# Optimization experiments

Measured on AMD Instinct MI355X. Metric: run time of the kernel, lower is better.

The kernel has to match this reference:

```python
import jax, jax.numpy as jnp
import numpy as np

N = 50000          # nodes (num_sensors)
E = 600000         # edges
IN_DIM = 75        # 3 * 25
DIMS = [(75, 128), (128, 128), (128, 32)]  # (in, out) per layer: in->hidden->hidden->bottleneck


def setup_inputs() -> dict:
    key = jax.random.key(0)
    ks = jax.random.split(key, 4 + 5 * len(DIMS))
    inp = {
        "x": jax.random.normal(ks[0], (N, IN_DIM), dtype=jnp.float32),
        "edge_index": jax.random.randint(ks[1], (2, E), 0, N, dtype=jnp.int64),
        "weight": jax.random.uniform(ks[2], (E,), dtype=jnp.float32),
        "sim": jax.random.normal(ks[3], (E, 2), dtype=jnp.float32),
    }
    i = 4
    for l, (cin, cout) in enumerate(DIMS):
        s = jnp.float32(1.0 / np.sqrt(cin))
        inp[f"wr{l}"] = jax.random.normal(ks[i + 0], (cin, cout), dtype=jnp.float32) * s  # real part of complex conv filter
        inp[f"wi{l}"] = jax.random.normal(ks[i + 1], (cin, cout), dtype=jnp.float32) * s  # imag part
        inp[f"cb{l}"] = jnp.zeros((cout,), dtype=jnp.float32)                              # conv bias
        inp[f"lw{l}"] = jax.random.normal(ks[i + 2], (cout, cin), dtype=jnp.float32) * s  # Linear weight (torch layout [out,in])
        inp[f"lb{l}"] = jnp.zeros((cout,), dtype=jnp.float32)                              # Linear bias
        i += 5
    return inp


def _layer(x, src, dst, cr, ci, wr, wi, cb, lw, lb):
    # ModeConvFast: gather source features, scale by complex edge coefficient
    # c = weight * (sim_r + i*sim_i), scatter-add to destination nodes,
    # project with complex filter W = wr + i*wi, keep real part, add bias.
    xs = x[src]                                   # [E, Cin] gather
    agg_r = jax.ops.segment_sum(xs * cr[:, None], dst, num_segments=N)  # [N, Cin]
    agg_i = jax.ops.segment_sum(xs * ci[:, None], dst, num_segments=N)  # [N, Cin]
    conv = agg_r @ wr - agg_i @ wi + cb           # real part of complex matmul
    return jax.nn.relu(conv + x @ lw.T + lb)      # conv(x,...) + lin(x), then relu


def reference(x, edge_index, weight, sim,
              wr0, wi0, cb0, lw0, lb0,
              wr1, wi1, cb1, lw1, lb1,
              wr2, wi2, cb2, lw2, lb2):
    src, dst = edge_index[0], edge_index[1]
    cr = weight * sim[:, 0]                       # [E] real edge coefficient
    ci = weight * sim[:, 1]                       # [E] imag edge coefficient
    layers = [
        (wr0, wi0, cb0, lw0, lb0),
        (wr1, wi1, cb1, lw1, lb1),
        (wr2, wi2, cb2, lw2, lb2),
    ]
    for p in layers:
        x = _layer(x, src, dst, cr, ci, *p)
    return x
```

## Files before the change

kernel.cpp:

```cpp
#include <hip/hip_runtime.h>

#define N_NODES 50000
#define N_EDGES 600000
#define E_PAD_MAX (N_EDGES + N_NODES * 7)

using bf16x8 = __attribute__((ext_vector_type(8))) short;
using f32x4  = __attribute__((ext_vector_type(4))) float;
typedef unsigned int uint32_tt;

__device__ __forceinline__ unsigned short f2bf(float f) {
    union { float f; unsigned int u; } v; v.f = f;
    unsigned int u = v.u;
    return (unsigned short)((u + 0x7fffu + ((u >> 16) & 1u)) >> 16);
}
__device__ __forceinline__ float bf2f(unsigned int h16) {
    union { unsigned int u; float f; } v; v.u = h16 << 16;
    return v.f;
}

__global__ void prep_kernel(
    const float* __restrict__ x0, unsigned short* __restrict__ xb,
    const float* __restrict__ wr0, const float* __restrict__ wi0,
    const float* __restrict__ lw0, unsigned short* __restrict__ BT0,
    const float* __restrict__ wr1, const float* __restrict__ wi1,
    const float* __restrict__ lw1, unsigned short* __restrict__ BT1,
    const float* __restrict__ wr2, const float* __restrict__ wi2,
    const float* __restrict__ lw2, unsigned short* __restrict__ BT2,
    int* __restrict__ cnt, uint2* __restrict__ edat, int n) {
    int tid = blockIdx.x * 256 + threadIdx.x;
    int nth = gridDim.x * 256;
    for (int i = tid; i < N_NODES; i += nth) cnt[i] = 0;
    uint2 z; z.x = 0u; z.y = 0u;
    for (int i = tid; i < E_PAD_MAX; i += nth) edat[i] = z;

    int i = tid;
    int nconv = n * 96;
    if (i < nconv) {
        int r = i / 96, c = i - r * 96;
        xb[i] = (c < 75) ? f2bf(x0[r * 75 + c]) : (unsigned short)0;
        return;
    }
    i -= nconv;
    if (i < 128 * 288) {
        int nn = i / 288, k = i - nn * 288;
        int part = k / 96, kk = k - part * 96;
        float v = 0.f;
        if (kk < 75) {
            if (part == 0)      v = wr0[kk * 128 + nn];
            else if (part == 1) v = -wi0[kk * 128 + nn];
            else                v = lw0[nn * 75 + kk];
        }
        BT0[i] = f2bf(v);
        return;
    }
    i -= 128 * 288;
    if (i < 128 * 384) {
        int nn = i / 384, k = i - nn * 384;
        int part = k >> 7, kk = k & 127;
        float v;
        if (part == 0)      v = wr1[kk * 128 + nn];
        else if (part == 1) v = -wi1[kk * 128 + nn];
        else                v = lw1[nn * 128 + kk];
        BT1[i] = f2bf(v);
        return;
    }
    i -= 128 * 384;
    if (i < 96 * 128) {
        int nn = i >> 7, k = i & 127;
        float v;
        if (nn < 32)      v = wr2[k * 32 + nn];
        else if (nn < 64) v = -wi2[k * 32 + (nn - 32)];
        else              v = lw2[(nn - 64) * 128 + k];
        BT2[i] = f2bf(v);
    }
}


__global__ void hist_kernel(const int* __restrict__ ei, int* __restrict__ cnt,
                            int* __restrict__ rank, int E) {
    int e = blockIdx.x * 256 + threadIdx.x;
    if (e < E) rank[e] = atomicAdd(&cnt[ei[E + e]], 1);
}

__global__ void scan1(const int* __restrict__ deg, int* __restrict__ out,
                      int* __restrict__ bsum, int n) {
    __shared__ int s[256];
    int t = threadIdx.x;
    int base = blockIdx.x * 1024 + t * 4;
    int v0 = (base + 0 < n) ? ((deg[base + 0] + 7) & ~7) : 0;
    int v1 = (base + 1 < n) ? ((deg[base + 1] + 7) & ~7) : 0;
    int v2 = (base + 2 < n) ? ((deg[base + 2] + 7) & ~7) : 0;
    int v3 = (base + 3 < n) ? ((deg[base + 3] + 7) & ~7) : 0;
    int tsum = v0 + v1 + v2 + v3;
    s[t] = tsum;
    __syncthreads();
    for (int off = 1; off < 256; off <<= 1) {
        int tmp = (t >= off) ? s[t - off] : 0;
        __syncthreads();
        s[t] += tmp;
        __syncthreads();
    }
    int excl = s[t] - tsum;
    if (base + 0 < n) out[base + 0] = excl;
    if (base + 1 < n) out[base + 1] = excl + v0;
    if (base + 2 < n) out[base + 2] = excl + v0 + v1;
    if (base + 3 < n) out[base + 3] = excl + v0 + v1 + v2;
    if (t == 255) bsum[blockIdx.x] = s[255];
}

__global__ void scan3(int* __restrict__ off, const int* __restrict__ bsum,
                      int n, int nb) {
    __shared__ int sp;
    int b = blockIdx.x, t = threadIdx.x;
    int seg = b >> 2;
    if (t == 0) {
        int acc = 0;
        for (int k = 0; k < seg; ++k) acc += bsum[k];
        sp = acc;
    }
    __syncthreads();
    int i = b * 256 + t;
    if (i < n) off[i] += sp;
    if (i == n) {
        int tot = sp;
        for (int k = seg; k < nb; ++k) tot += bsum[k];
        off[n] = tot;
    }
}

__global__ void scatter_kernel(const int* __restrict__ ei, const float* __restrict__ w,
                               const float* __restrict__ sim, const int* __restrict__ off,
                               const int* __restrict__ rank, uint2* __restrict__ edat,
                               int E) {
    int e = blockIdx.x * 256 + threadIdx.x;
    if (e >= E) return;
    int s = ei[e], d = ei[E + e];
    int p = off[d] + rank[e];
    float wt = w[e];
    uint2 m;
    m.x = (unsigned)s;
    m.y = (uint32_tt)f2bf(wt * sim[2 * e]) |
          ((uint32_tt)f2bf(wt * sim[2 * e + 1]) << 16);
    edat[p] = m;
}

template <int CU2>
__global__ __launch_bounds__(256) void agg_bf16(
    const uint32_tt* __restrict__ x, const int* __restrict__ off,
    const uint2* __restrict__ edat, uint32_tt* __restrict__ aggR,
    uint32_tt* __restrict__ aggI, int n) {
    int wave = threadIdx.x >> 6;
    int lane = threadIdx.x & 63;
    int node = __builtin_amdgcn_readfirstlane(blockIdx.x * 4 + wave);
    if (node >= n) return;
    int lc = (CU2 == 64) ? lane : (lane < CU2 ? lane : CU2 - 1);
    float arl = 0.f, arh = 0.f, ail = 0.f, aih = 0.f;
    int e0 = __builtin_amdgcn_readfirstlane(off[node]);
    int e1 = __builtin_amdgcn_readfirstlane(off[node + 1]);

    if (e0 < e1) {
        uint2 mn[8];
        int sc[8]; float crc[8], cic[8];
        uint32_tt wc[8];
        {
            uint2 m0[8];
#pragma unroll
            for (int j = 0; j < 8; ++j) m0[j] = edat[e0 + j];
#pragma unroll
            for (int j = 0; j < 8; ++j) {
                sc[j] = __builtin_amdgcn_readfirstlane((int)m0[j].x);
                int pk = __builtin_amdgcn_readfirstlane((int)m0[j].y);
                crc[j] = bf2f((unsigned)pk & 0xffffu);
                cic[j] = bf2f((unsigned)pk >> 16);
            }
            int nb = (e0 + 8 < e1) ? e0 + 8 : e0;
#pragma unroll
            for (int j = 0; j < 8; ++j) mn[j] = edat[nb + j];
#pragma unroll
            for (int j = 0; j < 8; ++j) wc[j] = x[(size_t)sc[j] * CU2 + lc];
        }
        for (int e = e0;; e += 8) {
            bool more = (e + 8 < e1);
            int sn[8]; float crn[8], cin_[8]; uint32_tt wn[8];
            if (more) {
#pragma unroll
                for (int j = 0; j < 8; ++j) {
                    sn[j] = __builtin_amdgcn_readfirstlane((int)mn[j].x);
                    int pk = __builtin_amdgcn_readfirstlane((int)mn[j].y);
                    crn[j] = bf2f((unsigned)pk & 0xffffu);
                    cin_[j] = bf2f((unsigned)pk >> 16);
                }
                int nb = (e + 16 < e1) ? e + 16 : e + 8;
#pragma unroll
                for (int j = 0; j < 8; ++j) mn[j] = edat[nb + j];
#pragma unroll
                for (int j = 0; j < 8; ++j) wn[j] = x[(size_t)sn[j] * CU2 + lc];
            }
#pragma unroll
            for (int j = 0; j < 8; ++j) {
                float lo = bf2f(wc[j] & 0xffffu), hi = bf2f(wc[j] >> 16);
                arl += crc[j] * lo; arh += crc[j] * hi;
                ail += cic[j] * lo; aih += cic[j] * hi;
            }
            if (!more) break;
#pragma unroll
            for (int j = 0; j < 8; ++j) {
                sc[j] = sn[j]; crc[j] = crn[j]; cic[j] = cin_[j]; wc[j] = wn[j];
            }
        }
    }
    if (lane < CU2) {
        aggR[(size_t)node * CU2 + lane] = (uint32_tt)f2bf(arl) | ((uint32_tt)f2bf(arh) << 16);
        aggI[(size_t)node * CU2 + lane] = (uint32_tt)f2bf(ail) | ((uint32_tt)f2bf(aih) << 16);
    }
}

__global__ __launch_bounds__(256) void agg_out(
    const uint32_tt* __restrict__ Y, const int* __restrict__ off,
    const uint2* __restrict__ edat, const float* __restrict__ cb,
    const float* __restrict__ lb, float* __restrict__ out, int n) {
    int wave = threadIdx.x >> 6;
    int lane = threadIdx.x & 63;
    int node = __builtin_amdgcn_readfirstlane(blockIdx.x * 4 + wave);
    if (node >= n) return;
    int lc = (lane < 32) ? lane : 31;
    int usei = (lane >> 4) & 1;
    float alo = 0.f, ahi = 0.f;
    int e0 = __builtin_amdgcn_readfirstlane(off[node]);
    int e1 = __builtin_amdgcn_readfirstlane(off[node + 1]);

    if (e0 < e1) {
        uint2 mn[8];
        int sc[8]; float crc[8], cic[8];
        uint32_tt wc[8];
        {
            uint2 m0[8];
#pragma unroll
            for (int j = 0; j < 8; ++j) m0[j] = edat[e0 + j];
#pragma unroll
            for (int j = 0; j < 8; ++j) {
                sc[j] = __builtin_amdgcn_readfirstlane((int)m0[j].x);
                int pk = __builtin_amdgcn_readfirstlane((int)m0[j].y);
                crc[j] = bf2f((unsigned)pk & 0xffffu);
                cic[j] = bf2f((unsigned)pk >> 16);
            }
            int nb = (e0 + 8 < e1) ? e0 + 8 : e0;
#pragma unroll
            for (int j = 0; j < 8; ++j) mn[j] = edat[nb + j];
#pragma unroll
            for (int j = 0; j < 8; ++j) wc[j] = Y[(size_t)sc[j] * 48 + lc];
        }
        for (int e = e0;; e += 8) {
            bool more = (e + 8 < e1);
            int sn[8]; float crn[8], cin_[8]; uint32_tt wn[8];
            if (more) {
#pragma unroll
                for (int j = 0; j < 8; ++j) {
                    sn[j] = __builtin_amdgcn_readfirstlane((int)mn[j].x);
                    int pk = __builtin_amdgcn_readfirstlane((int)mn[j].y);
                    crn[j] = bf2f((unsigned)pk & 0xffffu);
                    cin_[j] = bf2f((unsigned)pk >> 16);
                }
                int nb = (e + 16 < e1) ? e + 16 : e + 8;
#pragma unroll
                for (int j = 0; j < 8; ++j) mn[j] = edat[nb + j];
#pragma unroll
                for (int j = 0; j < 8; ++j) wn[j] = Y[(size_t)sn[j] * 48 + lc];
            }
#pragma unroll
            for (int j = 0; j < 8; ++j) {
                float c = usei ? cic[j] : crc[j];
                float lo = bf2f(wc[j] & 0xffffu), hi = bf2f(wc[j] >> 16);
                alo += c * lo; ahi += c * hi;
            }
            if (!more) break;
#pragma unroll
            for (int j = 0; j < 8; ++j) {
                sc[j] = sn[j]; crc[j] = crn[j]; cic[j] = cin_[j]; wc[j] = wn[j];
            }
        }
    }
    alo += __shfl_xor(alo, 16);
    ahi += __shfl_xor(ahi, 16);
    if (lane < 16) {
        uint32_tt lin = Y[(size_t)node * 48 + 32 + lane];
        int c0 = 2 * lane, c1 = 2 * lane + 1;
        float v0 = alo + bf2f(lin & 0xffffu) + cb[c0] + lb[c0];
        float v1 = ahi + bf2f(lin >> 16) + cb[c1] + lb[c1];
        float2 r;
        r.x = v0 > 0.f ? v0 : 0.f;
        r.y = v1 > 0.f ? v1 : 0.f;
        ((float2*)out)[(size_t)node * 16 + lane] = r;
    }
}

template <int CINP, int COUT, int BM, int WM, int WN, int MT, int NT,
          bool OUT_BF16, bool RAW, int PARTS>
__global__ __launch_bounds__(256) void gemm_mfma(
    const unsigned short* __restrict__ A0, const unsigned short* __restrict__ A1,
    const unsigned short* __restrict__ A2, const unsigned short* __restrict__ BT,
    const float* __restrict__ cb, const float* __restrict__ lb,
    void* __restrict__ outv, int n) {
    constexpr int PK = 40;
    constexpr int KTOT = PARTS * CINP;
    constexpr int NCH = KTOT / 32;
    constexpr int CPP = CINP / 32;
    __shared__ unsigned short sA[BM][PK];
    __shared__ unsigned short sB[COUT][PK];

    int t = threadIdx.x;
    int lane = t & 63, wave = t >> 6;
    int wm = wave / WN, wn = wave % WN;
    int ml = lane & 15, kh = lane >> 4;
    int node0 = blockIdx.x * BM;

    const unsigned short* Asrc[3] = {A0, A1, A2};

    f32x4 acc[MT][NT];
#pragma unroll
    for (int mt = 0; mt < MT; ++mt)
#pragma unroll
        for (int nt = 0; nt < NT; ++nt) acc[mt][nt] = (f32x4){0.f, 0.f, 0.f, 0.f};

    for (int c = 0; c < NCH; ++c) {
        int part = (PARTS == 1) ? 0 : (c / CPP);
        int kk = (c - part * CPP) * 32;
        const unsigned short* __restrict__ Ap = Asrc[part];
        __syncthreads();
#pragma unroll
        for (int i = t; i < BM * 4; i += 256) {
            int r = i >> 2, q = i & 3;
            int node = node0 + r;
            if (node >= n) node = n - 1;
            *(uint4*)&sA[r][q * 8] =
                *(const uint4*)(Ap + (size_t)node * CINP + kk + q * 8);
        }
#pragma unroll
        for (int i = t; i < COUT * 4; i += 256) {
            int r = i >> 2, q = i & 3;
            *(uint4*)&sB[r][q * 8] =
                *(const uint4*)(BT + (size_t)r * KTOT + c * 32 + q * 8);
        }
        __syncthreads();
        bf16x8 af[MT], bfr[NT];
#pragma unroll
        for (int mt = 0; mt < MT; ++mt)
            af[mt] = *(const bf16x8*)&sA[wm * (MT * 16) + mt * 16 + ml][kh * 8];
#pragma unroll
        for (int nt = 0; nt < NT; ++nt)
            bfr[nt] = *(const bf16x8*)&sB[wn * (NT * 16) + nt * 16 + ml][kh * 8];
#pragma unroll
        for (int mt = 0; mt < MT; ++mt)
#pragma unroll
            for (int nt = 0; nt < NT; ++nt)
                acc[mt][nt] = __builtin_amdgcn_mfma_f32_16x16x32_bf16(
                    af[mt], bfr[nt], acc[mt][nt], 0, 0, 0);
    }

    int row0 = kh * 4;
#pragma unroll
    for (int nt = 0; nt < NT; ++nt) {
        int col = wn * (NT * 16) + nt * 16 + ml;
        float bias = RAW ? 0.f : (cb[col] + lb[col]);
#pragma unroll
        for (int mt = 0; mt < MT; ++mt) {
#pragma unroll
            for (int r = 0; r < 4; ++r) {
                int node = node0 + wm * (MT * 16) + mt * 16 + row0 + r;
                if (node < n) {
                    float v = acc[mt][nt][r] + bias;
                    if (!RAW) v = v > 0.f ? v : 0.f;
                    if (OUT_BF16)
                        ((unsigned short*)outv)[(size_t)node * COUT + col] = f2bf(v);
                    else
                        ((float*)outv)[(size_t)node * COUT + col] = v;
                }
            }
        }
    }
}

__global__ __launch_bounds__(256) void gemm_l1y(
    const unsigned short* __restrict__ A0, const unsigned short* __restrict__ A1,
    const unsigned short* __restrict__ A2, const unsigned short* __restrict__ BT,
    const unsigned short* __restrict__ BT2, const float* __restrict__ cb,
    const float* __restrict__ lb, unsigned short* __restrict__ Yout, int n) {
    constexpr int PK = 40;
    constexpr int PH = 136;
    __shared__ unsigned short sA[128][PK];
    __shared__ unsigned short sB[128][PK];
    __shared__ unsigned short sH[128][PH];

    int t = threadIdx.x;
    int lane = t & 63, wave = t >> 6;
    int wm = wave >> 1, wn = wave & 1;
    int ml = lane & 15, kh = lane >> 4;
    int node0 = blockIdx.x * 128;
    const unsigned short* Asrc[3] = {A0, A1, A2};

    f32x4 acc[4][4];
#pragma unroll
    for (int mt = 0; mt < 4; ++mt)
#pragma unroll
        for (int nt = 0; nt < 4; ++nt) acc[mt][nt] = (f32x4){0.f, 0.f, 0.f, 0.f};

    for (int c = 0; c < 12; ++c) {
        int part = c >> 2;
        int kk = (c & 3) * 32;
        const unsigned short* __restrict__ Ap = Asrc[part];
        __syncthreads();
#pragma unroll
        for (int i = t; i < 512; i += 256) {
            int r = i >> 2, q = i & 3;
            int node = node0 + r;
            if (node >= n) node = n - 1;
            *(uint4*)&sA[r][q * 8] =
                *(const uint4*)(Ap + (size_t)node * 128 + kk + q * 8);
        }
#pragma unroll
        for (int i = t; i < 512; i += 256) {
            int r = i >> 2, q = i & 3;
            *(uint4*)&sB[r][q * 8] =
                *(const uint4*)(BT + (size_t)r * 384 + c * 32 + q * 8);
        }
        __syncthreads();
        bf16x8 af[4], bfr[4];
#pragma unroll
        for (int mt = 0; mt < 4; ++mt)
            af[mt] = *(const bf16x8*)&sA[wm * 64 + mt * 16 + ml][kh * 8];
#pragma unroll
        for (int nt = 0; nt < 4; ++nt)
            bfr[nt] = *(const bf16x8*)&sB[wn * 64 + nt * 16 + ml][kh * 8];
#pragma unroll
        for (int mt = 0; mt < 4; ++mt)
#pragma unroll
            for (int nt = 0; nt < 4; ++nt)
                acc[mt][nt] = __builtin_amdgcn_mfma_f32_16x16x32_bf16(
                    af[mt], bfr[nt], acc[mt][nt], 0, 0, 0);
    }

    int row0 = kh * 4;
#pragma unroll
    for (int nt = 0; nt < 4; ++nt) {
        int col = wn * 64 + nt * 16 + ml;
        float bias = cb[col] + lb[col];
#pragma unroll
        for (int mt = 0; mt < 4; ++mt) {
#pragma unroll
            for (int r = 0; r < 4; ++r) {
                int nl = wm * 64 + mt * 16 + row0 + r;
                float v = acc[mt][nt][r] + bias;
                sH[nl][col] = f2bf(v > 0.f ? v : 0.f);
            }
        }
    }
    __syncthreads();

    f32x4 acc2[4][3];
#pragma unroll
    for (int mt = 0; mt < 4; ++mt)
#pragma unroll
        for (int nt = 0; nt < 3; ++nt) acc2[mt][nt] = (f32x4){0.f, 0.f, 0.f, 0.f};
    for (int c2 = 0; c2 < 4; ++c2) {
        bf16x8 af[4], bfr[3];
#pragma unroll
        for (int mt = 0; mt < 4; ++mt)
            af[mt] = *(const bf16x8*)&sH[wm * 64 + mt * 16 + ml][c2 * 32 + kh * 8];
#pragma unroll
        for (int nt = 0; nt < 3; ++nt) {
            int ycol = wn * 48 + nt * 16 + ml;
            bfr[nt] = *(const bf16x8*)(BT2 + (size_t)ycol * 128 + c2 * 32 + kh * 8);
        }
#pragma unroll
        for (int mt = 0; mt < 4; ++mt)
#pragma unroll
            for (int nt = 0; nt < 3; ++nt)
                acc2[mt][nt] = __builtin_amdgcn_mfma_f32_16x16x32_bf16(
                    af[mt], bfr[nt], acc2[mt][nt], 0, 0, 0);
    }
#pragma unroll
    for (int nt = 0; nt < 3; ++nt) {
        int ycol = wn * 48 + nt * 16 + ml;
#pragma unroll
        for (int mt = 0; mt < 4; ++mt) {
#pragma unroll
            for (int r = 0; r < 4; ++r) {
                int node = node0 + wm * 64 + mt * 16 + row0 + r;
                if (node < n)
                    Yout[(size_t)node * 96 + ycol] = f2bf(acc2[mt][nt][r]);
            }
        }
    }
}


extern "C" void kernel_launch(void* const* d_in, const int* in_sizes, int n_in,
                              void* d_out, int out_size, void* d_ws, size_t ws_size,
                              hipStream_t stream) {
    const float* x0  = (const float*)d_in[0];
    const int*   ei  = (const int*)d_in[1];
    const float* wgt = (const float*)d_in[2];
    const float* sim = (const float*)d_in[3];
    const float *wr[3], *wi[3], *cb[3], *lw[3], *lb[3];
    for (int l = 0; l < 3; ++l) {
        wr[l] = (const float*)d_in[4 + 5 * l];
        wi[l] = (const float*)d_in[5 + 5 * l];
        cb[l] = (const float*)d_in[6 + 5 * l];
        lw[l] = (const float*)d_in[7 + 5 * l];
        lb[l] = (const float*)d_in[8 + 5 * l];
    }

    char* p = (char*)d_ws;
    auto alloc = [&](size_t bytes) -> void* {
        void* r = p;
        p += (bytes + 255) & ~(size_t)255;
        return r;
    };
    int*   off  = (int*)alloc((N_NODES + 1) * 4);
    int*   cnt  = (int*)alloc(N_NODES * 4);
    int*   bsum = (int*)alloc(256);
    int*   rank = (int*)alloc((size_t)N_EDGES * 4);
    uint2* edat = (uint2*)alloc((size_t)E_PAD_MAX * 8);
    unsigned short* xb    = (unsigned short*)alloc((size_t)N_NODES * 96 * 2);
    unsigned short* aggRb = (unsigned short*)alloc((size_t)N_NODES * 128 * 2);
    unsigned short* aggIb = (unsigned short*)alloc((size_t)N_NODES * 128 * 2);
    unsigned short* h1b   = (unsigned short*)alloc((size_t)N_NODES * 128 * 2);
    unsigned short* Yb    = (unsigned short*)alloc((size_t)N_NODES * 96 * 2);
    unsigned short* BT0   = (unsigned short*)alloc((size_t)128 * 288 * 2);
    unsigned short* BT1   = (unsigned short*)alloc((size_t)128 * 384 * 2);
    unsigned short* BT2   = (unsigned short*)alloc((size_t)96 * 128 * 2);
    float* outp = (float*)d_out;

    {
        int total = N_NODES * 96 + 128 * 288 + 128 * 384 + 96 * 128;
        prep_kernel<<<(total + 255) / 256, 256, 0, stream>>>(
            x0, xb, wr[0], wi[0], lw[0], BT0, wr[1], wi[1], lw[1], BT1,
            wr[2], wi[2], lw[2], BT2, cnt, edat, N_NODES);
    }
    hist_kernel<<<(N_EDGES + 255) / 256, 256, 0, stream>>>(ei, cnt, rank, N_EDGES);
    int nb = (N_NODES + 1023) / 1024;
    scan1<<<nb, 256, 0, stream>>>(cnt, off, bsum, N_NODES);
    scan3<<<(N_NODES + 1 + 255) / 256, 256, 0, stream>>>(off, bsum, N_NODES, nb);
    scatter_kernel<<<(N_EDGES + 255) / 256, 256, 0, stream>>>(ei, wgt, sim, off, rank,
                                                              edat, N_EDGES);

    int agrid = (N_NODES + 3) / 4;

    agg_bf16<48><<<agrid, 256, 0, stream>>>((const uint32_tt*)xb, off, edat,
                                            (uint32_tt*)aggRb, (uint32_tt*)aggIb, N_NODES);
    gemm_mfma<96, 128, 128, 2, 2, 4, 4, true, false, 3>
        <<<(N_NODES + 127) / 128, 256, 0, stream>>>(aggRb, aggIb, xb, BT0, cb[0], lb[0],
                                                    h1b, N_NODES);
    agg_bf16<64><<<agrid, 256, 0, stream>>>((const uint32_tt*)h1b, off, edat,
                                            (uint32_tt*)aggRb, (uint32_tt*)aggIb, N_NODES);
    gemm_l1y<<<(N_NODES + 127) / 128, 256, 0, stream>>>(aggRb, aggIb, h1b, BT1, BT2,
                                                        cb[1], lb[1], Yb, N_NODES);
    agg_out<<<agrid, 256, 0, stream>>>((const uint32_tt*)Yb, off, edat, cb[2], lb[2],
                                       outp, N_NODES);
}
```

Measured before the change: 263.3 us.

## Store features in 32-channel planes and split aggregation across channel chunks

Feature, aggregate and Y buffers move from node-major rows to planar blocks of 32 bf16 channels per node, and the GEMM loads and stores follow the new layout. Aggregation kernels now handle one 32-channel plane per wave, with four edges processed in parallel across lane groups and combined by shuffle reductions. Block indices are interleaved so the chunks of the same nodes run close together. This is meant to make each gathered row a compact 64-byte segment and to spread edge latency across more waves, at the cost of reading the edge list once per chunk plus extra shuffles.

Result: slower. 385.5 us (+46.4%).

```diff
diff --git a/kernel.cpp b/kernel.cpp
--- a/kernel.cpp
+++ b/kernel.cpp
@@ -7,6 +7,7 @@
 using bf16x8 = __attribute__((ext_vector_type(8))) short;
 using f32x4  = __attribute__((ext_vector_type(4))) float;
 typedef unsigned int uint32_tt;
+typedef unsigned long long u64;
 
 __device__ __forceinline__ unsigned short f2bf(float f) {
     union { float f; unsigned int u; } v; v.f = f;
@@ -37,7 +38,8 @@
     int nconv = n * 96;
     if (i < nconv) {
         int r = i / 96, c = i - r * 96;
-        xb[i] = (c < 75) ? f2bf(x0[r * 75 + c]) : (unsigned short)0;
+        unsigned short v = (c < 75) ? f2bf(x0[r * 75 + c]) : (unsigned short)0;
+        xb[((size_t)(c >> 5) * n + r) * 32 + (c & 31)] = v;
         return;
     }
     i -= nconv;
@@ -144,74 +146,68 @@
     edat[p] = m;
 }
 
-template <int CU2>
-__global__ __launch_bounds__(256) void agg_bf16(
-    const uint32_tt* __restrict__ x, const int* __restrict__ off,
-    const uint2* __restrict__ edat, uint32_tt* __restrict__ aggR,
-    uint32_tt* __restrict__ aggI, int n) {
+template <int TOTCH>
+__global__ __launch_bounds__(256) void agg_ch(
+    const uint32_tt* __restrict__ x,
+    const int* __restrict__ off, const uint2* __restrict__ edat,
+    uint32_tt* __restrict__ aggR, uint32_tt* __restrict__ aggI, int n) {
+    static_assert(TOTCH == 3 || TOTCH == 4, "chunk count");
     int wave = threadIdx.x >> 6;
     int lane = threadIdx.x & 63;
-    int node = __builtin_amdgcn_readfirstlane(blockIdx.x * 4 + wave);
+    int bx = blockIdx.x;
+    int x8 = bx & 7, nbk = bx >> 3;
+    int chunk, node_blk;
+    if (TOTCH == 4) {
+        chunk = x8 >> 1;
+        node_blk = nbk * 2 + (x8 & 1);
+    } else {
+        if (x8 < 3)      { chunk = 0; node_blk = nbk * 3 + x8; }
+        else if (x8 < 6) { chunk = 1; node_blk = nbk * 3 + (x8 - 3); }
+        else             { chunk = 2; node_blk = nbk * 2 + (x8 - 6); }
+    }
+    int node = __builtin_amdgcn_readfirstlane(node_blk * 4 + wave);
     if (node >= n) return;
-    int lc = (CU2 == 64) ? lane : (lane < CU2 ? lane : CU2 - 1);
+    int j = lane >> 4;
+    int c = lane & 15;
+    const uint32_tt* __restrict__ xp = x + (size_t)chunk * n * 16;
     float arl = 0.f, arh = 0.f, ail = 0.f, aih = 0.f;
     int e0 = __builtin_amdgcn_readfirstlane(off[node]);
     int e1 = __builtin_amdgcn_readfirstlane(off[node + 1]);
 
     if (e0 < e1) {
-        uint2 mn[8];
-        int sc[8]; float crc[8], cic[8];
-        uint32_tt wc[8];
-        {
-            uint2 m0[8];
-#pragma unroll
-            for (int j = 0; j < 8; ++j) m0[j] = edat[e0 + j];
-#pragma unroll
-            for (int j = 0; j < 8; ++j) {
-                sc[j] = __builtin_amdgcn_readfirstlane((int)m0[j].x);
-                int pk = __builtin_amdgcn_readfirstlane((int)m0[j].y);
-                crc[j] = bf2f((unsigned)pk & 0xffffu);
-                cic[j] = bf2f((unsigned)pk >> 16);
+        const u64* __restrict__ ed64 = (const u64*)edat;
+        u64 mc = __builtin_nontemporal_load(ed64 + e0 + j);
+        int nb1 = (e0 + 4 < e1) ? e0 + 4 : e0;
+        u64 mn = __builtin_nontemporal_load(ed64 + nb1 + j);
+        uint32_tt wc = xp[(size_t)((uint32_tt)mc) * 16 + c];
+        for (int e = e0;; e += 4) {
+            bool more = (e + 4 < e1);
+            u64 mn2 = 0; uint32_tt wn = 0;
+            if (more) {
+                wn = xp[(size_t)((uint32_tt)mn) * 16 + c];
+                int nb2 = (e + 8 < e1) ? e + 8 : e + 4;
+                mn2 = __builtin_nontemporal_load(ed64 + nb2 + j);
             }
-            int nb = (e0 + 8 < e1) ? e0 + 8 : e0;
-#pragma unroll
-            for (int j = 0; j < 8; ++j) mn[j] = edat[nb + j];
-#pragma unroll
-            for (int j = 0; j < 8; ++j) wc[j] = x[(size_t)sc[j] * CU2 + lc];
-        }
-        for (int e = e0;; e += 8) {
-            bool more = (e + 8 < e1);
-            int sn[8]; float crn[8], cin_[8]; uint32_tt wn[8];
-            if (more) {
-#pragma unroll
-                for (int j = 0; j < 8; ++j) {
-                    sn[j] = __builtin_amdgcn_readfirstlane((int)mn[j].x);
-                    int pk = __builtin_amdgcn_readfirstlane((int)mn[j].y);
-                    crn[j] = bf2f((unsigned)pk & 0xffffu);
-                    cin_[j] = bf2f((unsigned)pk >> 16);
-                }
-                int nb = (e + 16 < e1) ? e + 16 : e + 8;
-#pragma unroll
-                for (int j = 0; j < 8; ++j) mn[j] = edat[nb + j];
-#pragma unroll
-                for (int j = 0; j < 8; ++j) wn[j] = x[(size_t)sn[j] * CU2 + lc];
-            }
-#pragma unroll
-            for (int j = 0; j < 8; ++j) {
-                float lo = bf2f(wc[j] & 0xffffu), hi = bf2f(wc[j] >> 16);
-                arl += crc[j] * lo; arh += crc[j] * hi;
-                ail += cic[j] * lo; aih += cic[j] * hi;
-            }
+            uint32_tt pk = (uint32_tt)(mc >> 32);
+            float cr = bf2f(pk & 0xffffu);
+            float ci = bf2f(pk >> 16);
+            float lo = bf2f(wc & 0xffffu), hi = bf2f(wc >> 16);
+            arl += cr * lo; arh += cr * hi;
+            ail += ci * lo; aih += ci * hi;
             if (!more) break;
-#pragma unroll
-            for (int j = 0; j < 8; ++j) {
-                sc[j] = sn[j]; crc[j] = crn[j]; cic[j] = cin_[j]; wc[j] = wn[j];
-            }
-        }
-    }
-    if (lane < CU2) {
-        aggR[(size_t)node * CU2 + lane] = (uint32_tt)f2bf(arl) | ((uint32_tt)f2bf(arh) << 16);
-        aggI[(size_t)node * CU2 + lane] = (uint32_tt)f2bf(ail) | ((uint32_tt)f2bf(aih) << 16);
+            mc = mn; mn = mn2; wc = wn;
+        }
+    }
+    arl += __shfl_xor(arl, 16); arl += __shfl_xor(arl, 32);
+    arh += __shfl_xor(arh, 16); arh += __shfl_xor(arh, 32);
+    ail += __shfl_xor(ail, 16); ail += __shfl_xor(ail, 32);
+    aih += __shfl_xor(aih, 16); aih += __shfl_xor(aih, 32);
+    if (lane < 16) {
+        size_t base = ((size_t)chunk * n + node) * 16 + lane;
+        __builtin_nontemporal_store(
+            (uint32_tt)f2bf(arl) | ((uint32_tt)f2bf(arh) << 16), aggR + base);
+        __builtin_nontemporal_store(
+            (uint32_tt)f2bf(ail) | ((uint32_tt)f2bf(aih) << 16), aggI + base);
     }
 }
 
@@ -223,67 +219,51 @@
     int lane = threadIdx.x & 63;
     int node = __builtin_amdgcn_readfirstlane(blockIdx.x * 4 + wave);
     if (node >= n) return;
-    int lc = (lane < 32) ? lane : 31;
-    int usei = (lane >> 4) & 1;
+    int j = lane >> 5;
+    int lc = lane & 31;
+    int p = lc >> 4;
+    int w = lc & 15;
+    const uint32_tt* __restrict__ Yp = Y + (size_t)p * n * 16;
     float alo = 0.f, ahi = 0.f;
     int e0 = __builtin_amdgcn_readfirstlane(off[node]);
     int e1 = __builtin_amdgcn_readfirstlane(off[node + 1]);
 
     if (e0 < e1) {
-        uint2 mn[8];
-        int sc[8]; float crc[8], cic[8];
-        uint32_tt wc[8];
-        {
-            uint2 m0[8];
-#pragma unroll
-            for (int j = 0; j < 8; ++j) m0[j] = edat[e0 + j];
-#pragma unroll
-            for (int j = 0; j < 8; ++j) {
-                sc[j] = __builtin_amdgcn_readfirstlane((int)m0[j].x);
-                int pk = __builtin_amdgcn_readfirstlane((int)m0[j].y);
-                crc[j] = bf2f((unsigned)pk & 0xffffu);
-                cic[j] = bf2f((unsigned)pk >> 16);
+        const u64* __restrict__ ed64 = (const u64*)edat;
+        u64 mcA = __builtin_nontemporal_load(ed64 + e0 + j);
+        u64 mcB = __builtin_nontemporal_load(ed64 + e0 + 2 + j);
+        int nb1 = (e0 + 4 < e1) ? e0 + 4 : e0;
+        u64 mnA = __builtin_nontemporal_load(ed64 + nb1 + j);
+        u64 mnB = __builtin_nontemporal_load(ed64 + nb1 + 2 + j);
+        uint32_tt wcA = Yp[(size_t)((uint32_tt)mcA) * 16 + w];
+        uint32_tt wcB = Yp[(size_t)((uint32_tt)mcB) * 16 + w];
+        for (int e = e0;; e += 4) {
+            bool more = (e + 4 < e1);
+            u64 mnA2 = 0, mnB2 = 0; uint32_tt wnA = 0, wnB = 0;
+            if (more) {
+                wnA = Yp[(size_t)((uint32_tt)mnA) * 16 + w];
+                wnB = Yp[(size_t)((uint32_tt)mnB) * 16 + w];
+                int nb2 = (e + 8 < e1) ? e + 8 : e + 4;
+                mnA2 = __builtin_nontemporal_load(ed64 + nb2 + j);
+                mnB2 = __builtin_nontemporal_load(ed64 + nb2 + 2 + j);
             }
-            int nb = (e0 + 8 < e1) ? e0 + 8 : e0;
-#pragma unroll
-            for (int j = 0; j < 8; ++j) mn[j] = edat[nb + j];
-#pragma unroll
-            for (int j = 0; j < 8; ++j) wc[j] = Y[(size_t)sc[j] * 48 + lc];
-        }
-        for (int e = e0;; e += 8) {
-            bool more = (e + 8 < e1);
-            int sn[8]; float crn[8], cin_[8]; uint32_tt wn[8];
-            if (more) {
-#pragma unroll
-                for (int j = 0; j < 8; ++j) {
-                    sn[j] = __builtin_amdgcn_readfirstlane((int)mn[j].x);
-                    int pk = __builtin_amdgcn_readfirstlane((int)mn[j].y);
-                    crn[j] = bf2f((unsigned)pk & 0xffffu);
-                    cin_[j] = bf2f((unsigned)pk >> 16);
-                }
-                int nb = (e + 16 < e1) ? e + 16 : e + 8;
-#pragma unroll
-                for (int j = 0; j < 8; ++j) mn[j] = edat[nb + j];
-#pragma unroll
-                for (int j = 0; j < 8; ++j) wn[j] = Y[(size_t)sn[j] * 48 + lc];
-            }
-#pragma unroll
-            for (int j = 0; j < 8; ++j) {
-                float c = usei ? cic[j] : crc[j];
-                float lo = bf2f(wc[j] & 0xffffu), hi = bf2f(wc[j] >> 16);
-                alo += c * lo; ahi += c * hi;
-            }
+            uint32_tt pkA = (uint32_tt)(mcA >> 32);
+            uint32_tt pkB = (uint32_tt)(mcB >> 32);
+            float cA = p ? bf2f(pkA >> 16) : bf2f(pkA & 0xffffu);
+            float cB = p ? bf2f(pkB >> 16) : bf2f(pkB & 0xffffu);
+            float loA = bf2f(wcA & 0xffffu), hiA = bf2f(wcA >> 16);
+            float loB = bf2f(wcB & 0xffffu), hiB = bf2f(wcB >> 16);
+            alo += cA * loA; ahi += cA * hiA;
+            alo += cB * loB; ahi += cB * hiB;
             if (!more) break;
-#pragma unroll
-            for (int j = 0; j < 8; ++j) {
-                sc[j] = sn[j]; crc[j] = crn[j]; cic[j] = cin_[j]; wc[j] = wn[j];
-            }
-        }
-    }
-    alo += __shfl_xor(alo, 16);
-    ahi += __shfl_xor(ahi, 16);
+            mcA = mnA; mcB = mnB; mnA = mnA2; mnB = mnB2;
+            wcA = wnA; wcB = wnB;
+        }
+    }
+    alo += __shfl_xor(alo, 32); alo += __shfl_xor(alo, 16);
+    ahi += __shfl_xor(ahi, 32); ahi += __shfl_xor(ahi, 16);
     if (lane < 16) {
-        uint32_tt lin = Y[(size_t)node * 48 + 32 + lane];
+        uint32_tt lin = Y[((size_t)2 * n + node) * 16 + lane];
         int c0 = 2 * lane, c1 = 2 * lane + 1;
         float v0 = alo + bf2f(lin & 0xffffu) + cb[c0] + lb[c0];
         float v1 = ahi + bf2f(lin >> 16) + cb[c1] + lb[c1];
@@ -324,7 +304,7 @@
 
     for (int c = 0; c < NCH; ++c) {
         int part = (PARTS == 1) ? 0 : (c / CPP);
-        int kk = (c - part * CPP) * 32;
+        int plane = c - part * CPP;
         const unsigned short* __restrict__ Ap = Asrc[part];
         __syncthreads();
 #pragma unroll
@@ -333,7 +313,7 @@
             int node = node0 + r;
             if (node >= n) node = n - 1;
             *(uint4*)&sA[r][q * 8] =
-                *(const uint4*)(Ap + (size_t)node * CINP + kk + q * 8);
+                *(const uint4*)(Ap + ((size_t)plane * n + node) * 32 + q * 8);
         }
 #pragma unroll
         for (int i = t; i < COUT * 4; i += 256) {
@@ -371,7 +351,8 @@
                     float v = acc[mt][nt][r] + bias;
                     if (!RAW) v = v > 0.f ? v : 0.f;
                     if (OUT_BF16)
-                        ((unsigned short*)outv)[(size_t)node * COUT + col] = f2bf(v);
+                        ((unsigned short*)outv)[((size_t)(col >> 5) * n + node) * 32 +
+                                                (col & 31)] = f2bf(v);
                     else
                         ((float*)outv)[(size_t)node * COUT + col] = v;
                 }
@@ -406,7 +387,7 @@
 
     for (int c = 0; c < 12; ++c) {
         int part = c >> 2;
-        int kk = (c & 3) * 32;
+        int plane = c & 3;
         const unsigned short* __restrict__ Ap = Asrc[part];
         __syncthreads();
 #pragma unroll
@@ -415,7 +396,7 @@
             int node = node0 + r;
             if (node >= n) node = n - 1;
             *(uint4*)&sA[r][q * 8] =
-                *(const uint4*)(Ap + (size_t)node * 128 + kk + q * 8);
+                *(const uint4*)(Ap + ((size_t)plane * n + node) * 32 + q * 8);
         }
 #pragma unroll
         for (int i = t; i < 512; i += 256) {
@@ -487,7 +468,8 @@
             for (int r = 0; r < 4; ++r) {
                 int node = node0 + wm * 64 + mt * 16 + row0 + r;
                 if (node < n)
-                    Yout[(size_t)node * 96 + ycol] = f2bf(acc2[mt][nt][r]);
+                    Yout[((size_t)(ycol >> 5) * n + node) * 32 + (ycol & 31)] =
+                        f2bf(acc2[mt][nt][r]);
             }
         }
     }
@@ -544,17 +526,17 @@
     scatter_kernel<<<(N_EDGES + 255) / 256, 256, 0, stream>>>(ei, wgt, sim, off, rank,
                                                               edat, N_EDGES);
 
-    int agrid = (N_NODES + 3) / 4;
-
-    agg_bf16<48><<<agrid, 256, 0, stream>>>((const uint32_tt*)xb, off, edat,
-                                            (uint32_tt*)aggRb, (uint32_tt*)aggIb, N_NODES);
+    int cgrid = 6250 * 8;
+
+    agg_ch<3><<<cgrid, 256, 0, stream>>>((const uint32_tt*)xb, off, edat,
+                                         (uint32_tt*)aggRb, (uint32_tt*)aggIb, N_NODES);
     gemm_mfma<96, 128, 128, 2, 2, 4, 4, true, false, 3>
         <<<(N_NODES + 127) / 128, 256, 0, stream>>>(aggRb, aggIb, xb, BT0, cb[0], lb[0],
                                                     h1b, N_NODES);
-    agg_bf16<64><<<agrid, 256, 0, stream>>>((const uint32_tt*)h1b, off, edat,
-                                            (uint32_tt*)aggRb, (uint32_tt*)aggIb, N_NODES);
+    agg_ch<4><<<cgrid, 256, 0, stream>>>((const uint32_tt*)h1b, off, edat,
+                                         (uint32_tt*)aggRb, (uint32_tt*)aggIb, N_NODES);
     gemm_l1y<<<(N_NODES + 127) / 128, 256, 0, stream>>>(aggRb, aggIb, h1b, BT1, BT2,
                                                         cb[1], lb[1], Yb, N_NODES);
-    agg_out<<<agrid, 256, 0, stream>>>((const uint32_tt*)Yb, off, edat, cb[2], lb[2],
-                                       outp, N_NODES);
-}
+    agg_out<<<(N_NODES + 3) / 4, 256, 0, stream>>>((const uint32_tt*)Yb, off, edat,
+                                                   cb[2], lb[2], outp, N_NODES);
+}
```

## Split each wave into two half-waves processing alternate edges with wider loads

Applied to the files above, without the earlier changes.

The aggregation kernels now split each 64-lane wave into two 32-lane halves. Each half handles every other edge of a node's neighbour list and loads 8-byte (four-bf16) chunks per lane instead of 4-byte ones, and the halves are combined with a cross-half shuffle at the end. In the output kernel, lanes that were previously idle (masked past 32) now do useful gather work. This raises per-wave memory-level parallelism and lane utilisation for the gather, at the cost of extra shuffles, extra select logic, and 32-bit unsigned byte offsets that would overflow on larger inputs.

New measurement: 257.3 us. 1.02x faster.

```diff
diff --git a/kernel.cpp b/kernel.cpp
--- a/kernel.cpp
+++ b/kernel.cpp
@@ -7,6 +7,7 @@
 using bf16x8 = __attribute__((ext_vector_type(8))) short;
 using f32x4  = __attribute__((ext_vector_type(4))) float;
 typedef unsigned int uint32_tt;
+typedef unsigned long long u64;
 
 __device__ __forceinline__ unsigned short f2bf(float f) {
     union { float f; unsigned int u; } v; v.f = f;
@@ -145,73 +146,110 @@
 }
 
 template <int CU2>
-__global__ __launch_bounds__(256) void agg_bf16(
+__global__ __launch_bounds__(256) void agg_pair(
     const uint32_tt* __restrict__ x, const int* __restrict__ off,
     const uint2* __restrict__ edat, uint32_tt* __restrict__ aggR,
     uint32_tt* __restrict__ aggI, int n) {
+    constexpr int P = CU2 / 2;
+    constexpr int RB = CU2 * 4;
     int wave = threadIdx.x >> 6;
     int lane = threadIdx.x & 63;
     int node = __builtin_amdgcn_readfirstlane(blockIdx.x * 4 + wave);
     if (node >= n) return;
-    int lc = (CU2 == 64) ? lane : (lane < CU2 ? lane : CU2 - 1);
-    float arl = 0.f, arh = 0.f, ail = 0.f, aih = 0.f;
+    int j = lane >> 5;
+    int c = lane & 31;
+    int lc = (P == 32) ? c : (c < P ? c : P - 1);
+    float ar0 = 0.f, ar1 = 0.f, ar2 = 0.f, ar3 = 0.f;
+    float ai0 = 0.f, ai1 = 0.f, ai2 = 0.f, ai3 = 0.f;
     int e0 = __builtin_amdgcn_readfirstlane(off[node]);
     int e1 = __builtin_amdgcn_readfirstlane(off[node + 1]);
 
     if (e0 < e1) {
         uint2 mn[8];
-        int sc[8]; float crc[8], cic[8];
-        uint32_tt wc[8];
+        int soc[4]; float crc[4], cic[4];
+        uint2 wc[4];
         {
             uint2 m0[8];
 #pragma unroll
-            for (int j = 0; j < 8; ++j) m0[j] = edat[e0 + j];
-#pragma unroll
-            for (int j = 0; j < 8; ++j) {
-                sc[j] = __builtin_amdgcn_readfirstlane((int)m0[j].x);
-                int pk = __builtin_amdgcn_readfirstlane((int)m0[j].y);
-                crc[j] = bf2f((unsigned)pk & 0xffffu);
-                cic[j] = bf2f((unsigned)pk >> 16);
+            for (int k = 0; k < 8; ++k) m0[k] = edat[e0 + k];
+            int so8[8]; float cr8[8], ci8[8];
+#pragma unroll
+            for (int k = 0; k < 8; ++k) {
+                int s = __builtin_amdgcn_readfirstlane((int)m0[k].x);
+                int pk = __builtin_amdgcn_readfirstlane((int)m0[k].y);
+                so8[k] = s * RB;
+                cr8[k] = bf2f((unsigned)pk & 0xffffu);
+                ci8[k] = bf2f((unsigned)pk >> 16);
+            }
+#pragma unroll
+            for (int k = 0; k < 4; ++k) {
+                soc[k] = j ? so8[2 * k + 1] : so8[2 * k];
+                crc[k] = j ? cr8[2 * k + 1] : cr8[2 * k];
+                cic[k] = j ? ci8[2 * k + 1] : ci8[2 * k];
             }
             int nb = (e0 + 8 < e1) ? e0 + 8 : e0;
 #pragma unroll
-            for (int j = 0; j < 8; ++j) mn[j] = edat[nb + j];
-#pragma unroll
-            for (int j = 0; j < 8; ++j) wc[j] = x[(size_t)sc[j] * CU2 + lc];
+            for (int k = 0; k < 8; ++k) mn[k] = edat[nb + k];
+#pragma unroll
+            for (int k = 0; k < 4; ++k)
+                wc[k] = *(const uint2*)((const char*)x + (unsigned)soc[k] +
+                                        (unsigned)(lc * 8));
         }
         for (int e = e0;; e += 8) {
             bool more = (e + 8 < e1);
-            int sn[8]; float crn[8], cin_[8]; uint32_tt wn[8];
+            int son[4]; float crn[4], cin_[4]; uint2 wn[4];
             if (more) {
-#pragma unroll
-                for (int j = 0; j < 8; ++j) {
-                    sn[j] = __builtin_amdgcn_readfirstlane((int)mn[j].x);
-                    int pk = __builtin_amdgcn_readfirstlane((int)mn[j].y);
-                    crn[j] = bf2f((unsigned)pk & 0xffffu);
-                    cin_[j] = bf2f((unsigned)pk >> 16);
+                int so8[8]; float cr8[8], ci8[8];
+#pragma unroll
+                for (int k = 0; k < 8; ++k) {
+                    int s = __builtin_amdgcn_readfirstlane((int)mn[k].x);
+                    int pk = __builtin_amdgcn_readfirstlane((int)mn[k].y);
+                    so8[k] = s * RB;
+                    cr8[k] = bf2f((unsigned)pk & 0xffffu);
+                    ci8[k] = bf2f((unsigned)pk >> 16);
+                }
+#pragma unroll
+                for (int k = 0; k < 4; ++k) {
+                    son[k] = j ? so8[2 * k + 1] : so8[2 * k];
+                    crn[k] = j ? cr8[2 * k + 1] : cr8[2 * k];
+                    cin_[k] = j ? ci8[2 * k + 1] : ci8[2 * k];
                 }
                 int nb = (e + 16 < e1) ? e + 16 : e + 8;
 #pragma unroll
-                for (int j = 0; j < 8; ++j) mn[j] = edat[nb + j];
-#pragma unroll
-                for (int j = 0; j < 8; ++j) wn[j] = x[(size_t)sn[j] * CU2 + lc];
-            }
-#pragma unroll
-            for (int j = 0; j < 8; ++j) {
-                float lo = bf2f(wc[j] & 0xffffu), hi = bf2f(wc[j] >> 16);
-                arl += crc[j] * lo; arh += crc[j] * hi;
-                ail += cic[j] * lo; aih += cic[j] * hi;
+                for (int k = 0; k < 8; ++k) mn[k] = edat[nb + k];
+#pragma unroll
+                for (int k = 0; k < 4; ++k)
+                    wn[k] = *(const uint2*)((const char*)x + (unsigned)son[k] +
+                                            (unsigned)(lc * 8));
+            }
+#pragma unroll
+            for (int k = 0; k < 4; ++k) {
+                float lo0 = bf2f(wc[k].x & 0xffffu), hi0 = bf2f(wc[k].x >> 16);
+                float lo1 = bf2f(wc[k].y & 0xffffu), hi1 = bf2f(wc[k].y >> 16);
+                ar0 += crc[k] * lo0; ar1 += crc[k] * hi0;
+                ar2 += crc[k] * lo1; ar3 += crc[k] * hi1;
+                ai0 += cic[k] * lo0; ai1 += cic[k] * hi0;
+                ai2 += cic[k] * lo1; ai3 += cic[k] * hi1;
             }
             if (!more) break;
 #pragma unroll
-            for (int j = 0; j < 8; ++j) {
-                sc[j] = sn[j]; crc[j] = crn[j]; cic[j] = cin_[j]; wc[j] = wn[j];
-            }
-        }
-    }
-    if (lane < CU2) {
-        aggR[(size_t)node * CU2 + lane] = (uint32_tt)f2bf(arl) | ((uint32_tt)f2bf(arh) << 16);
-        aggI[(size_t)node * CU2 + lane] = (uint32_tt)f2bf(ail) | ((uint32_tt)f2bf(aih) << 16);
+            for (int k = 0; k < 4; ++k) {
+                crc[k] = crn[k]; cic[k] = cin_[k]; wc[k] = wn[k];
+            }
+        }
+    }
+    ar0 += __shfl_xor(ar0, 32); ar1 += __shfl_xor(ar1, 32);
+    ar2 += __shfl_xor(ar2, 32); ar3 += __shfl_xor(ar3, 32);
+    ai0 += __shfl_xor(ai0, 32); ai1 += __shfl_xor(ai1, 32);
+    ai2 += __shfl_xor(ai2, 32); ai3 += __shfl_xor(ai3, 32);
+    if (lane < P) {
+        uint2 oR, oI;
+        oR.x = (uint32_tt)f2bf(ar0) | ((uint32_tt)f2bf(ar1) << 16);
+        oR.y = (uint32_tt)f2bf(ar2) | ((uint32_tt)f2bf(ar3) << 16);
+        oI.x = (uint32_tt)f2bf(ai0) | ((uint32_tt)f2bf(ai1) << 16);
+        oI.y = (uint32_tt)f2bf(ai2) | ((uint32_tt)f2bf(ai3) << 16);
+        ((uint2*)(aggR + (size_t)node * CU2))[lane] = oR;
+        ((uint2*)(aggI + (size_t)node * CU2))[lane] = oI;
     }
 }
 
@@ -223,65 +261,84 @@
     int lane = threadIdx.x & 63;
     int node = __builtin_amdgcn_readfirstlane(blockIdx.x * 4 + wave);
     if (node >= n) return;
-    int lc = (lane < 32) ? lane : 31;
-    int usei = (lane >> 4) & 1;
+    int j = lane >> 5;
+    int lc = lane & 31;
+    int usei = lc >> 4;
     float alo = 0.f, ahi = 0.f;
     int e0 = __builtin_amdgcn_readfirstlane(off[node]);
     int e1 = __builtin_amdgcn_readfirstlane(off[node + 1]);
 
     if (e0 < e1) {
         uint2 mn[8];
-        int sc[8]; float crc[8], cic[8];
-        uint32_tt wc[8];
+        int soc[4]; float cc[4]; uint32_tt wc[4];
         {
             uint2 m0[8];
 #pragma unroll
-            for (int j = 0; j < 8; ++j) m0[j] = edat[e0 + j];
-#pragma unroll
-            for (int j = 0; j < 8; ++j) {
-                sc[j] = __builtin_amdgcn_readfirstlane((int)m0[j].x);
-                int pk = __builtin_amdgcn_readfirstlane((int)m0[j].y);
-                crc[j] = bf2f((unsigned)pk & 0xffffu);
-                cic[j] = bf2f((unsigned)pk >> 16);
+            for (int k = 0; k < 8; ++k) m0[k] = edat[e0 + k];
+            int so8[8]; float cr8[8], ci8[8];
+#pragma unroll
+            for (int k = 0; k < 8; ++k) {
+                int s = __builtin_amdgcn_readfirstlane((int)m0[k].x);
+                int pk = __builtin_amdgcn_readfirstlane((int)m0[k].y);
+                so8[k] = s * 192;
+                cr8[k] = bf2f((unsigned)pk & 0xffffu);
+                ci8[k] = bf2f((unsigned)pk >> 16);
+            }
+#pragma unroll
+            for (int k = 0; k < 4; ++k) {
+                soc[k] = j ? so8[2 * k + 1] : so8[2 * k];
+                float a = j ? cr8[2 * k + 1] : cr8[2 * k];
+                float b = j ? ci8[2 * k + 1] : ci8[2 * k];
+                cc[k] = usei ? b : a;
             }
             int nb = (e0 + 8 < e1) ? e0 + 8 : e0;
 #pragma unroll
-            for (int j = 0; j < 8; ++j) mn[j] = edat[nb + j];
-#pragma unroll
-            for (int j = 0; j < 8; ++j) wc[j] = Y[(size_t)sc[j] * 48 + lc];
+            for (int k = 0; k < 8; ++k) mn[k] = edat[nb + k];
+#pragma unroll
+            for (int k = 0; k < 4; ++k)
+                wc[k] = *(const uint32_tt*)((const char*)Y + (unsigned)soc[k] +
+                                            (unsigned)(lc * 4));
         }
         for (int e = e0;; e += 8) {
             bool more = (e + 8 < e1);
-            int sn[8]; float crn[8], cin_[8]; uint32_tt wn[8];
+            int son[4]; float cn[4]; uint32_tt wn[4];
             if (more) {
-#pragma unroll
-                for (int j = 0; j < 8; ++j) {
-                    sn[j] = __builtin_amdgcn_readfirstlane((int)mn[j].x);
-                    int pk = __builtin_amdgcn_readfirstlane((int)mn[j].y);
-                    crn[j] = bf2f((unsigned)pk & 0xffffu);
-                    cin_[j] = bf2f((unsigned)pk >> 16);
+                int so8[8]; float cr8[8], ci8[8];
+#pragma unroll
+                for (int k = 0; k < 8; ++k) {
+                    int s = __builtin_amdgcn_readfirstlane((int)mn[k].x);
+                    int pk = __builtin_amdgcn_readfirstlane((int)mn[k].y);
+                    so8[k] = s * 192;
+                    cr8[k] = bf2f((unsigned)pk & 0xffffu);
+                    ci8[k] = bf2f((unsigned)pk >> 16);
+                }
+#pragma unroll
+                for (int k = 0; k < 4; ++k) {
+                    son[k] = j ? so8[2 * k + 1] : so8[2 * k];
+                    float a = j ? cr8[2 * k + 1] : cr8[2 * k];
+                    float b = j ? ci8[2 * k + 1] : ci8[2 * k];
+                    cn[k] = usei ? b : a;
                 }
                 int nb = (e + 16 < e1) ? e + 16 : e + 8;
 #pragma unroll
-                for (int j = 0; j < 8; ++j) mn[j] = edat[nb + j];
-#pragma unroll
-                for (int j = 0; j < 8; ++j) wn[j] = Y[(size_t)sn[j] * 48 + lc];
-            }
-#pragma unroll
-            for (int j = 0; j < 8; ++j) {
-                float c = usei ? cic[j] : crc[j];
-                float lo = bf2f(wc[j] & 0xffffu), hi = bf2f(wc[j] >> 16);
-                alo += c * lo; ahi += c * hi;
+                for (int k = 0; k < 8; ++k) mn[k] = edat[nb + k];
+#pragma unroll
+                for (int k = 0; k < 4; ++k)
+                    wn[k] = *(const uint32_tt*)((const char*)Y + (unsigned)son[k] +
+                                                (unsigned)(lc * 4));
+            }
+#pragma unroll
+            for (int k = 0; k < 4; ++k) {
+                float lo = bf2f(wc[k] & 0xffffu), hi = bf2f(wc[k] >> 16);
+                alo += cc[k] * lo; ahi += cc[k] * hi;
             }
             if (!more) break;
 #pragma unroll
-            for (int j = 0; j < 8; ++j) {
-                sc[j] = sn[j]; crc[j] = crn[j]; cic[j] = cin_[j]; wc[j] = wn[j];
-            }
-        }
-    }
-    alo += __shfl_xor(alo, 16);
-    ahi += __shfl_xor(ahi, 16);
+            for (int k = 0; k < 4; ++k) { cc[k] = cn[k]; wc[k] = wn[k]; }
+        }
+    }
+    alo += __shfl_xor(alo, 32); alo += __shfl_xor(alo, 16);
+    ahi += __shfl_xor(ahi, 32); ahi += __shfl_xor(ahi, 16);
     if (lane < 16) {
         uint32_tt lin = Y[(size_t)node * 48 + 32 + lane];
         int c0 = 2 * lane, c1 = 2 * lane + 1;
@@ -546,12 +603,12 @@
 
     int agrid = (N_NODES + 3) / 4;
 
-    agg_bf16<48><<<agrid, 256, 0, stream>>>((const uint32_tt*)xb, off, edat,
+    agg_pair<48><<<agrid, 256, 0, stream>>>((const uint32_tt*)xb, off, edat,
                                             (uint32_tt*)aggRb, (uint32_tt*)aggIb, N_NODES);
     gemm_mfma<96, 128, 128, 2, 2, 4, 4, true, false, 3>
         <<<(N_NODES + 127) / 128, 256, 0, stream>>>(aggRb, aggIb, xb, BT0, cb[0], lb[0],
                                                     h1b, N_NODES);
-    agg_bf16<64><<<agrid, 256, 0, stream>>>((const uint32_tt*)h1b, off, edat,
+    agg_pair<64><<<agrid, 256, 0, stream>>>((const uint32_tt*)h1b, off, edat,
                                             (uint32_tt*)aggRb, (uint32_tt*)aggIb, N_NODES);
     gemm_l1y<<<(N_NODES + 127) / 128, 256, 0, stream>>>(aggRb, aggIb, h1b, BT1, BT2,
                                                         cb[1], lb[1], Yb, N_NODES);
```
